# Kernel tuning notes

Measured on AMD Instinct MI355X. Metric: run time of the kernel, lower is better.

The kernel has to match this reference:

```python
import jax, jax.numpy as jnp
import numpy as np


def setup_inputs() -> dict:
    key = jax.random.key(0)
    ks = jax.random.split(key, 4)
    B, C, H, W = 16, 3, 256, 256
    n_steps, kO, k = 10, 2, 3
    CK = C * kO
    x = jax.random.normal(ks[0], (B, C, H, W), jnp.float32)
    kerK = jax.random.normal(ks[1], (n_steps, CK, 1, k, k), jnp.float32) * 0.3
    beta = jax.random.uniform(ks[2], (n_steps, 1, CK, 1, 1), jnp.float32, minval=0.01, maxval=0.1)
    rho = jax.random.uniform(ks[3], (n_steps, 1, CK, 1, 1), jnp.float32, minval=0.5, maxval=1.5)
    return {"x": x, "kerK": kerK, "beta": beta, "rho": rho}


def _dwconv(ker, x, pad):
    # depthwise 'same' cross-correlation (torch conv2d semantics)
    # ker: (CK,1,k,k), x: (B,CK,H,W) -> (B,CK,H,W)
    return jax.lax.conv_general_dilated(
        x, ker, (1, 1), [(pad, pad), (pad, pad)],
        dimension_numbers=("NCHW", "OIHW", "NCHW"),
        feature_group_count=x.shape[1])


def _psf2otf(ker, H, W):
    # ker: (C, kk, kk) with kk odd; shift center to origin, then FFT -> (C,H,W) complex
    C, kk, _ = ker.shape
    r = (kk - 1) // 2
    pad = jnp.zeros((C, H, W), ker.dtype).at[:, :kk, :kk].set(ker)
    pad = jnp.roll(pad, (-r, -r), axis=(-2, -1))
    return jnp.fft.fft2(pad)


def _tv_forward(x, kerK, beta, rho):
    B, C, H, W = x.shape
    n_steps, CK, _, k, _ = kerK.shape
    kO = CK // C
    kR = (k - 1) // 2
    f = x
    u = x                                        # state u init = input (loop(): u = x0)
    p = jnp.zeros((B, CK, H, W), x.dtype)        # auxiliary p ~= Du
    mu = jnp.zeros_like(p)                       # scaled multiplier
    for i in range(n_steps):                     # structural unroll over fixed n_steps
        K = kerK[i]                              # (CK,1,k,k)
        rh = rho[i]                              # (1,CK,1,1)
        gm = beta[i] / rho[i]                    # gamma = beta/rho (per step docstring)
        # kerW = rho * flip(K): adjoint D^T as correlation with flipped kernel
        kerW = rh.reshape(CK, 1, 1, 1) * K[:, :, ::-1, ::-1]
        # w1 = f + CKtoC(D^T (p - mu)); CKtoC sums groups of kO channels
        w1 = f + _dwconv(kerW, p - mu, kR).reshape(B, C, kO, H, W).sum(2)
        # K^T K: depthwise full autocorrelation of each kernel -> (CK, 2k-1, 2k-1)
        ktk = jax.lax.conv_general_dilated(
            K.transpose(1, 0, 2, 3), K, (1, 1), [(k - 1, k - 1)] * 2,
            dimension_numbers=("NCHW", "OIHW", "NCHW"),
            feature_group_count=CK)[0] * rh.reshape(CK, 1, 1)
        sktk = ktk.reshape(C, kO, 2 * k - 1, 2 * k - 1).sum(1)   # (C,kk,kk)
        kerH = sktk.at[:, k - 1, k - 1].add(1.0)                 # I + rho*K^T K
        otf = _psf2otf(kerH, H, W)                               # (C,H,W) complex
        # FFT Wiener-style solve: u = ifft( fft(w1) / OTF )
        u = jnp.fft.ifft2(jnp.fft.fft2(w1) / otf[None]).real
        # c = D u (depthwise corr on channel-repeated u)
        c = _dwconv(K, jnp.repeat(u, kO, axis=1), kR)
        v = c + mu
        p = jnp.sign(v) * jnp.maximum(jnp.abs(v) - gm, 0.0)      # soft-threshold
        mu = mu + c - p
    return u


def reference(x, kerK, beta, rho):
    return _tv_forward(x, kerK, beta, rho)
```

## Files before the change

### kernel.cpp

```cpp
#include <hip/hip_runtime.h>
#include <hip/hip_fp16.h>
#include <math.h>

#define BATCH 16
#define CH 3
#define CKCH 6
#define HH 256
#define WW 256
#define NSTEPS 10
#define SW 132
#define HSP (HH*SW)
#define IDX(i) ((i) ^ (((i) >> 4) & 15))

struct __align__(8) h4 { __half2 a, b; };

__device__ __forceinline__ float2 cmulf(float2 a, float2 b) {
  return make_float2(a.x * b.x - a.y * b.y, a.x * b.y + a.y * b.x);
}
__device__ __forceinline__ float4 h4tof4(h4 v) {
  float2 f0 = __half22float2(v.a), f1 = __half22float2(v.b);
  return make_float4(f0.x, f0.y, f1.x, f1.y);
}
__device__ __forceinline__ h4 f4toh4(float4 v) {
  h4 r;
  r.a = __float22half2_rn(make_float2(v.x, v.y));
  r.b = __float22half2_rn(make_float2(v.z, v.w));
  return r;
}

template <int INV, int STRIDE>
__device__ __forceinline__ void wave_fft256(float2* buf, const float2* tw, int l) {
  int pp = 0;
#pragma unroll
  for (int st = 0; st < 4; ++st) {
    int m = 1 << (2 * st);
    int r = l & (m - 1);
    int qm = l - r;
    float2 w1 = tw[qm], w2 = tw[qm + 64], w3 = tw[2 * qm];
    if (INV) { w1.y = -w1.y; w2.y = -w2.y; w3.y = -w3.y; }
    const float2* src = buf + pp * STRIDE;
    float2* dst = buf + (pp ^ 1) * STRIDE;
    float2 x0 = src[IDX(l)];
    float2 x1 = src[IDX(l + 128)];
    float2 x2 = src[IDX(l + 64)];
    float2 x3 = src[IDX(l + 192)];
    __builtin_amdgcn_wave_barrier();
    float2 aA = make_float2(x0.x + x1.x, x0.y + x1.y);
    float2 bA = cmulf(w1, make_float2(x0.x - x1.x, x0.y - x1.y));
    float2 aB = make_float2(x2.x + x3.x, x2.y + x3.y);
    float2 bB = cmulf(w2, make_float2(x2.x - x3.x, x2.y - x3.y));
    int base = 4 * qm + r;
    dst[IDX(base)]         = make_float2(aA.x + aB.x, aA.y + aB.y);
    dst[IDX(base + 2 * m)] = cmulf(w3, make_float2(aA.x - aB.x, aA.y - aB.y));
    dst[IDX(base + m)]     = make_float2(bA.x + bB.x, bA.y + bB.y);
    dst[IDX(base + 3 * m)] = cmulf(w3, make_float2(bA.x - bB.x, bA.y - bB.y));
    pp ^= 1;
    __builtin_amdgcn_wave_barrier();
  }
}

__global__ __launch_bounds__(256) void xcast_kernel(const float4* __restrict__ x,
                                                    h4* __restrict__ xh) {
  int i = blockIdx.x * 256 + threadIdx.x;
  xh[i] = f4toh4(x[i]);
}

__global__ __launch_bounds__(256) void hinv3_kernel(const float* __restrict__ kerK,
                                                    const float* __restrict__ rho,
                                                    float* __restrict__ HinvT) {
  int bid = blockIdx.x;
  int kx = bid % 129;
  int ic = bid / 129;
  int c = ic % CH, i = ic / CH;
  __shared__ float kerH[25];
  __shared__ float ctab[256];
  int tid = threadIdx.x;
  if (tid < 25) {
    int a = tid / 5, b = tid % 5;
    float s = (a == 2 && b == 2) ? 1.0f : 0.0f;
    for (int o = 0; o < 2; ++o) {
      int ck = c * 2 + o;
      const float* Kk = kerK + (i * CKCH + ck) * 9;
      float rh = rho[i * CKCH + ck];
      float ac = 0.f;
      for (int ty = 0; ty < 3; ++ty)
        for (int tx = 0; tx < 3; ++tx) {
          int ya = a - 2 + ty, xb = b - 2 + tx;
          if (ya >= 0 && ya < 3 && xb >= 0 && xb < 3)
            ac += Kk[ya * 3 + xb] * Kk[ty * 3 + tx];
        }
      s += rh * ac;
    }
    kerH[tid] = s;
  }
  ctab[tid] = cosf(6.283185307179586f * (float)tid / 256.0f);
  __syncthreads();
  int ky = tid;
  float acc = 0.f;
#pragma unroll
  for (int a = 0; a < 5; ++a)
#pragma unroll
    for (int b = 0; b < 5; ++b)
      acc += kerH[a * 5 + b] * ctab[(ky * (a - 2) + kx * (b - 2)) & 255];
  HinvT[((size_t)ic * 129 + kx) * 256 + ky] = 1.0f / (65536.0f * acc);
}

__global__ __launch_bounds__(256, 3) void bigstep_kernel(
    const __half* __restrict__ xh, const float* __restrict__ kerK,
    const float* __restrict__ beta, const float* __restrict__ rho,
    const __half2* __restrict__ specIn, const __half* __restrict__ muIn,
    __half* __restrict__ muOut, __half2* __restrict__ specOut,
    float* __restrict__ uout, int wstep) {
  int bid = blockIdx.x;
  int strip = bid & 31;
  int bc = bid >> 5;
  int c = bc % CH, b = bc / CH;
  int y0 = strip * 8;
  int tid = threadIdx.x;
  int u = tid >> 6, l = tid & 63;
  bool final_ = (wstep == 10);
  bool first = (wstep == 0);

  __shared__ float su[12][264];
  __shared__ float sd[2][10][264];
  __shared__ float2 zz[4][2][256];
  __shared__ float2 tw[128];

  if (tid < 128) {
    float sn, cs;
    sincosf(-6.283185307179586f * (float)tid / 256.0f, &sn, &cs);
    tw[tid] = make_float2(cs, sn);
  }
  __syncthreads();

  float2* Z = &zz[u][0][0];

  if (wstep >= 1) {
    int nround = final_ ? 1 : 2;
    for (int round = 0; round < nround; ++round) {
      int j = final_ ? (u + 1) : (round * 4 + u);
      bool act = (j < 6);
      int ya = y0 - 2 + 2 * j;
      if (act && ya >= 0 && ya < HH) {
        const __half2* Ar = specIn + ((size_t)bc * HH + ya) * SW;
        const __half2* Br = Ar + SW;
#pragma unroll
        for (int h = 0; h < 2; ++h) {
          int t = l + h * 64;
          float2 A = __half22float2(Ar[t]), B = __half22float2(Br[t]);
          Z[IDX(t)] = make_float2(A.x - B.y, A.y + B.x);
          int mI = 128 - t;
          float2 Am = __half22float2(Ar[mI]), Bm = __half22float2(Br[mI]);
          float2 zh;
          if (t == 0) zh = make_float2(Am.x - Bm.y, Am.y + Bm.x);
          else        zh = make_float2(Am.x + Bm.y, Bm.x - Am.y);
          Z[IDX(t + 128)] = zh;
        }
        __builtin_amdgcn_wave_barrier();
        wave_fft256<1, 256>(Z, tw, l);
        if (final_) {
          float* oa = uout + ((size_t)bc * HH + ya) * WW;
#pragma unroll
          for (int h = 0; h < 4; ++h) {
            int xx = l + h * 64;
            float2 z = Z[IDX(xx)];
            oa[xx] = z.x;
            oa[WW + xx] = z.y;
          }
        } else {
          int r0 = 2 * j;
#pragma unroll
          for (int h = 0; h < 4; ++h) {
            int xx = l + h * 64;
            float2 z = Z[IDX(xx)];
            su[r0][4 + xx] = z.x;
            su[r0 + 1][4 + xx] = z.y;
          }
        }
      } else if (act) {
        int r0 = 2 * j;
        for (int k2 = l; k2 < 264; k2 += 64) { su[r0][k2] = 0.f; su[r0 + 1][k2] = 0.f; }
      }
    }
  }
  if (final_) return;

  if (!first) {
    __syncthreads();
    bool muZero = (wstep == 1);
    int ps = wstep - 1;
#pragma unroll 1
    for (int it = 0; it < 5; ++it) {
      int task = it * 4 + u;
      int o = task / 10, rr = task % 10;
      int y = y0 - 1 + rr;
      int ck = c * 2 + o;
      float4 dq = make_float4(0.f, 0.f, 0.f, 0.f);
      if (y >= 0 && y < HH) {
        const float* Kp = kerK + (ps * CKCH + ck) * 9;
        float kk[9];
#pragma unroll
        for (int q = 0; q < 9; ++q) kk[q] = Kp[q];
        float gm = beta[ps * CKCH + ck] / rho[ps * CKCH + ck];
        float4 c4 = make_float4(0.f, 0.f, 0.f, 0.f);
#pragma unroll
        for (int dy = 0; dy < 3; ++dy) {
          float4 mid = *(const float4*)&su[rr + dy][4 + 4 * l];
          float lft = __shfl_up(mid.w, 1); if (l == 0) lft = 0.f;
          float rgt = __shfl_down(mid.x, 1); if (l == 63) rgt = 0.f;
          float w0 = kk[dy * 3], w1 = kk[dy * 3 + 1], w2 = kk[dy * 3 + 2];
          c4.x += w0 * lft   + w1 * mid.x + w2 * mid.y;
          c4.y += w0 * mid.x + w1 * mid.y + w2 * mid.z;
          c4.z += w0 * mid.y + w1 * mid.z + w2 * mid.w;
          c4.w += w0 * mid.z + w1 * mid.w + w2 * rgt;
        }
        size_t gidx = (((size_t)b * CKCH + ck) * HH + y) * WW + 4 * l;
        float4 m4 = make_float4(0.f, 0.f, 0.f, 0.f);
        if (!muZero) m4 = h4tof4(*(const h4*)(muIn + gidx));
        float4 mn4;
        {
          float v = c4.x + m4.x, av = fabsf(v) - gm;
          float pn = (av > 0.f) ? ((v > 0.f) ? av : -av) : 0.f;
          mn4.x = m4.x + c4.x - pn; dq.x = pn - mn4.x;
        }
        {
          float v = c4.y + m4.y, av = fabsf(v) - gm;
          float pn = (av > 0.f) ? ((v > 0.f) ? av : -av) : 0.f;
          mn4.y = m4.y + c4.y - pn; dq.y = pn - mn4.y;
        }
        {
          float v = c4.z + m4.z, av = fabsf(v) - gm;
          float pn = (av > 0.f) ? ((v > 0.f) ? av : -av) : 0.f;
          mn4.z = m4.z + c4.z - pn; dq.z = pn - mn4.z;
        }
        {
          float v = c4.w + m4.w, av = fabsf(v) - gm;
          float pn = (av > 0.f) ? ((v > 0.f) ? av : -av) : 0.f;
          mn4.w = m4.w + c4.w - pn; dq.w = pn - mn4.w;
        }
        if (rr >= 1 && rr <= 8) *(h4*)(muOut + gidx) = f4toh4(mn4);
      }
      *(float4*)&sd[o][rr][4 + 4 * l] = dq;
    }
  }
  __syncthreads();

  int ya = y0 + 2 * u;
  const h4* xa = (const h4*)(xh + ((size_t)(b * CH + c) * HH + ya) * WW);
  float4 va = h4tof4(xa[l]), vb = h4tof4(xa[64 + l]);
  if (!first) {
#pragma unroll
    for (int o = 0; o < 2; ++o) {
      int ck = c * 2 + o;
      float rh = rho[wstep * CKCH + ck];
      const float* Kk = kerK + (wstep * CKCH + ck) * 9;
      float kw[9];
#pragma unroll
      for (int dy = 0; dy < 3; ++dy)
#pragma unroll
        for (int dx = 0; dx < 3; ++dx)
          kw[dy * 3 + dx] = rh * Kk[(2 - dy) * 3 + (2 - dx)];
      float4 mid[4]; float lf[4], rg[4];
#pragma unroll
      for (int r4 = 0; r4 < 4; ++r4) {
        mid[r4] = *(const float4*)&sd[o][2 * u + r4][4 + 4 * l];
        lf[r4] = __shfl_up(mid[r4].w, 1); if (l == 0) lf[r4] = 0.f;
        rg[r4] = __shfl_down(mid[r4].x, 1); if (l == 63) rg[r4] = 0.f;
      }
#pragma unroll
      for (int dy = 0; dy < 3; ++dy) {
        float w0 = kw[dy * 3], w1 = kw[dy * 3 + 1], w2 = kw[dy * 3 + 2];
        va.x += w0 * lf[dy]     + w1 * mid[dy].x   + w2 * mid[dy].y;
        va.y += w0 * mid[dy].x  + w1 * mid[dy].y   + w2 * mid[dy].z;
        va.z += w0 * mid[dy].y  + w1 * mid[dy].z   + w2 * mid[dy].w;
        va.w += w0 * mid[dy].z  + w1 * mid[dy].w   + w2 * rg[dy];
        vb.x += w0 * lf[dy+1]    + w1 * mid[dy+1].x + w2 * mid[dy+1].y;
        vb.y += w0 * mid[dy+1].x + w1 * mid[dy+1].y + w2 * mid[dy+1].z;
        vb.z += w0 * mid[dy+1].y + w1 * mid[dy+1].z + w2 * mid[dy+1].w;
        vb.w += w0 * mid[dy+1].z + w1 * mid[dy+1].w + w2 * rg[dy+1];
      }
    }
  }
  Z[IDX(4 * l + 0)] = make_float2(va.x, vb.x);
  Z[IDX(4 * l + 1)] = make_float2(va.y, vb.y);
  Z[IDX(4 * l + 2)] = make_float2(va.z, vb.z);
  Z[IDX(4 * l + 3)] = make_float2(va.w, vb.w);
  __builtin_amdgcn_wave_barrier();
  wave_fft256<0, 256>(Z, tw, l);
  __half2* Sa = specOut + ((size_t)bc * HH + ya) * SW;
  __half2* Sb = Sa + SW;
#pragma unroll
  for (int h = 0; h < 2; ++h) {
    int k = l + h * 64;
    int mI = (256 - k) & 255;
    float2 zk = Z[IDX(k)], zm = Z[IDX(mI)];
    Sa[k] = __float22half2_rn(make_float2(0.5f * (zk.x + zm.x), 0.5f * (zk.y - zm.y)));
    Sb[k] = __float22half2_rn(make_float2(0.5f * (zk.y + zm.y), 0.5f * (zm.x - zk.x)));
  }
  if (l == 0) {
    float2 z1 = Z[IDX(128)];
    Sa[128] = __float22half2_rn(make_float2(z1.x, 0.f));
    Sb[128] = __float22half2_rn(make_float2(z1.y, 0.f));
  }
}

__global__ __launch_bounds__(256, 4) void colfft_kernel(__half2* __restrict__ spec,
                                                        const float* __restrict__ HinvT, int step) {
  int bid = blockIdx.x;
  int g = bid % 17;
  int bc = bid / 17;
  int c = bc % CH;
  int x0 = g * 8;
  __half2* f = spec + (size_t)bc * HSP;

  __shared__ float2 az[8][2][258];
  __shared__ float2 tw[128];
  int tid = threadIdx.x;
  if (tid < 128) {
    float sn, cs;
    sincosf(-6.283185307179586f * (float)tid / 256.0f, &sn, &cs);
    tw[tid] = make_float2(cs, sn);
  }
  for (int e = tid; e < 2048; e += 256) {
    int row = e >> 3, col = e & 7;
    int kx = x0 + col;
    if (kx <= 128) az[col][0][IDX(row)] = __half22float2(f[row * SW + kx]);
  }
  __syncthreads();

  int u = tid >> 6, l = tid & 63;
#pragma unroll
  for (int cc = 0; cc < 2; ++cc) {
    int col = 2 * u + cc;
    int kx = x0 + col;
    if (kx <= 128) {
      float2* A = &az[col][0][0];
      wave_fft256<0, 258>(A, tw, l);
      const float* T = HinvT + ((size_t)(step * CH + c) * 129 + kx) * 256;
#pragma unroll
      for (int h = 0; h < 4; ++h) {
        int idx = l + 64 * h;
        float tv = T[idx];
        float2 z = A[IDX(idx)];
        A[IDX(idx)] = make_float2(z.x * tv, z.y * tv);
      }
      __builtin_amdgcn_wave_barrier();
      wave_fft256<1, 258>(A, tw, l);
    }
  }
  __syncthreads();
  for (int e = tid; e < 2048; e += 256) {
    int row = e >> 3, col = e & 7;
    int kx = x0 + col;
    if (kx <= 128) f[row * SW + kx] = __float22half2_rn(az[col][0][IDX(row)]);
  }
}

extern "C" void kernel_launch(void* const* d_in, const int* in_sizes, int n_in,
                              void* d_out, int out_size, void* d_ws, size_t ws_size,
                              hipStream_t stream) {
  const float* x = (const float*)d_in[0];
  const float* kerK = (const float*)d_in[1];
  const float* beta = (const float*)d_in[2];
  const float* rho = (const float*)d_in[3];
  float* out = (float*)d_out;

  const size_t PMU = (size_t)BATCH * CKCH * HH * WW;
  const size_t SPL = (size_t)BATCH * CH * HSP;
  const size_t XN = (size_t)BATCH * CH * HH * WW;

  __half* muA = (__half*)d_ws;
  __half* muB = muA + PMU;
  __half2* specA = (__half2*)(muB + PMU);
  __half2* specB = specA + SPL;
  float* HinvT = (float*)(specB + SPL);
  __half* xh = (__half*)(HinvT + (size_t)30 * 129 * 256);

  xcast_kernel<<<XN / 1024, 256, 0, stream>>>((const float4*)x, (h4*)xh);
  hinv3_kernel<<<30 * 129, 256, 0, stream>>>(kerK, rho, HinvT);

  for (int i = 0; i < NSTEPS; ++i) {
    __half2* sIn = (i & 1) ? specA : specB;
    __half2* sOut = (i & 1) ? specB : specA;
    const __half* mi = (i & 1) ? muB : muA;
    __half* mo = (i & 1) ? muA : muB;
    bigstep_kernel<<<BATCH * CH * 32, 256, 0, stream>>>(
        xh, kerK, beta, rho, sIn, mi, mo, sOut, out, i);
    colfft_kernel<<<BATCH * CH * 17, 256, 0, stream>>>(sOut, HinvT, i);
  }
  bigstep_kernel<<<BATCH * CH * 32, 256, 0, stream>>>(
      xh, kerK, beta, rho, specB, muA, muB, specA, out, 10);
}
```

Before: 429.5 us.

## Shrink LDS footprint: in-place FFT, half-precision staging, one column per wave

The wave-level radix-4 FFT now works in place on a single buffer instead of ping-ponging between two, which halves the FFT scratch in both kernels. The bigstep kernel stores its u and dual staging tiles in LDS as fp16 and raises its occupancy hint. The column FFT kernel switches to 512-thread blocks with one column per wave. The aim is to cut LDS per block so more waves stay resident and hide latency, at the cost of extra fp16 rounding in intermediates. In-place updates rely on each lane reading all four inputs before the wave barrier and then writing.

```diff
diff --git a/kernel.cpp b/kernel.cpp
--- a/kernel.cpp
+++ b/kernel.cpp
@@ -28,9 +28,8 @@
   return r;
 }
 
-template <int INV, int STRIDE>
+template <int INV>
 __device__ __forceinline__ void wave_fft256(float2* buf, const float2* tw, int l) {
-  int pp = 0;
 #pragma unroll
   for (int st = 0; st < 4; ++st) {
     int m = 1 << (2 * st);
@@ -38,23 +37,20 @@
     int qm = l - r;
     float2 w1 = tw[qm], w2 = tw[qm + 64], w3 = tw[2 * qm];
     if (INV) { w1.y = -w1.y; w2.y = -w2.y; w3.y = -w3.y; }
-    const float2* src = buf + pp * STRIDE;
-    float2* dst = buf + (pp ^ 1) * STRIDE;
-    float2 x0 = src[IDX(l)];
-    float2 x1 = src[IDX(l + 128)];
-    float2 x2 = src[IDX(l + 64)];
-    float2 x3 = src[IDX(l + 192)];
+    float2 x0 = buf[IDX(l)];
+    float2 x1 = buf[IDX(l + 128)];
+    float2 x2 = buf[IDX(l + 64)];
+    float2 x3 = buf[IDX(l + 192)];
     __builtin_amdgcn_wave_barrier();
     float2 aA = make_float2(x0.x + x1.x, x0.y + x1.y);
     float2 bA = cmulf(w1, make_float2(x0.x - x1.x, x0.y - x1.y));
     float2 aB = make_float2(x2.x + x3.x, x2.y + x3.y);
     float2 bB = cmulf(w2, make_float2(x2.x - x3.x, x2.y - x3.y));
     int base = 4 * qm + r;
-    dst[IDX(base)]         = make_float2(aA.x + aB.x, aA.y + aB.y);
-    dst[IDX(base + 2 * m)] = cmulf(w3, make_float2(aA.x - aB.x, aA.y - aB.y));
-    dst[IDX(base + m)]     = make_float2(bA.x + bB.x, bA.y + bB.y);
-    dst[IDX(base + 3 * m)] = cmulf(w3, make_float2(bA.x - bB.x, bA.y - bB.y));
-    pp ^= 1;
+    buf[IDX(base)]         = make_float2(aA.x + aB.x, aA.y + aB.y);
+    buf[IDX(base + 2 * m)] = cmulf(w3, make_float2(aA.x - aB.x, aA.y - aB.y));
+    buf[IDX(base + m)]     = make_float2(bA.x + bB.x, bA.y + bB.y);
+    buf[IDX(base + 3 * m)] = cmulf(w3, make_float2(bA.x - bB.x, bA.y - bB.y));
     __builtin_amdgcn_wave_barrier();
   }
 }
@@ -105,7 +101,7 @@
   HinvT[((size_t)ic * 129 + kx) * 256 + ky] = 1.0f / (65536.0f * acc);
 }
 
-__global__ __launch_bounds__(256, 3) void bigstep_kernel(
+__global__ __launch_bounds__(256, 6) void bigstep_kernel(
     const __half* __restrict__ xh, const float* __restrict__ kerK,
     const float* __restrict__ beta, const float* __restrict__ rho,
     const __half2* __restrict__ specIn, const __half* __restrict__ muIn,
@@ -121,9 +117,9 @@
   bool final_ = (wstep == 10);
   bool first = (wstep == 0);
 
-  __shared__ float su[12][264];
-  __shared__ float sd[2][10][264];
-  __shared__ float2 zz[4][2][256];
+  __shared__ __half su[12][264];
+  __shared__ __half sdm[2][10][264];
+  __shared__ float2 zz[4][256];
   __shared__ float2 tw[128];
 
   if (tid < 128) {
@@ -133,7 +129,7 @@
   }
   __syncthreads();
 
-  float2* Z = &zz[u][0][0];
+  float2* Z = &zz[u][0];
 
   if (wstep >= 1) {
     int nround = final_ ? 1 : 2;
@@ -157,7 +153,7 @@
           Z[IDX(t + 128)] = zh;
         }
         __builtin_amdgcn_wave_barrier();
-        wave_fft256<1, 256>(Z, tw, l);
+        wave_fft256<1>(Z, tw, l);
         if (final_) {
           float* oa = uout + ((size_t)bc * HH + ya) * WW;
 #pragma unroll
@@ -173,13 +169,16 @@
           for (int h = 0; h < 4; ++h) {
             int xx = l + h * 64;
             float2 z = Z[IDX(xx)];
-            su[r0][4 + xx] = z.x;
-            su[r0 + 1][4 + xx] = z.y;
+            su[r0][4 + xx] = __float2half(z.x);
+            su[r0 + 1][4 + xx] = __float2half(z.y);
           }
         }
       } else if (act) {
         int r0 = 2 * j;
-        for (int k2 = l; k2 < 264; k2 += 64) { su[r0][k2] = 0.f; su[r0 + 1][k2] = 0.f; }
+        for (int k2 = l; k2 < 264; k2 += 64) {
+          su[r0][k2] = __float2half(0.f);
+          su[r0 + 1][k2] = __float2half(0.f);
+        }
       }
     }
   }
@@ -205,7 +204,7 @@
         float4 c4 = make_float4(0.f, 0.f, 0.f, 0.f);
 #pragma unroll
         for (int dy = 0; dy < 3; ++dy) {
-          float4 mid = *(const float4*)&su[rr + dy][4 + 4 * l];
+          float4 mid = h4tof4(*(const h4*)&su[rr + dy][4 + 4 * l]);
           float lft = __shfl_up(mid.w, 1); if (l == 0) lft = 0.f;
           float rgt = __shfl_down(mid.x, 1); if (l == 63) rgt = 0.f;
           float w0 = kk[dy * 3], w1 = kk[dy * 3 + 1], w2 = kk[dy * 3 + 2];
@@ -240,7 +239,7 @@
         }
         if (rr >= 1 && rr <= 8) *(h4*)(muOut + gidx) = f4toh4(mn4);
       }
-      *(float4*)&sd[o][rr][4 + 4 * l] = dq;
+      *(h4*)&sdm[o][rr][4 + 4 * l] = f4toh4(dq);
     }
   }
   __syncthreads();
@@ -263,7 +262,7 @@
       float4 mid[4]; float lf[4], rg[4];
 #pragma unroll
       for (int r4 = 0; r4 < 4; ++r4) {
-        mid[r4] = *(const float4*)&sd[o][2 * u + r4][4 + 4 * l];
+        mid[r4] = h4tof4(*(const h4*)&sdm[o][2 * u + r4][4 + 4 * l]);
         lf[r4] = __shfl_up(mid[r4].w, 1); if (l == 0) lf[r4] = 0.f;
         rg[r4] = __shfl_down(mid[r4].x, 1); if (l == 63) rg[r4] = 0.f;
       }
@@ -286,7 +285,7 @@
   Z[IDX(4 * l + 2)] = make_float2(va.z, vb.z);
   Z[IDX(4 * l + 3)] = make_float2(va.w, vb.w);
   __builtin_amdgcn_wave_barrier();
-  wave_fft256<0, 256>(Z, tw, l);
+  wave_fft256<0>(Z, tw, l);
   __half2* Sa = specOut + ((size_t)bc * HH + ya) * SW;
   __half2* Sb = Sa + SW;
 #pragma unroll
@@ -304,7 +303,7 @@
   }
 }
 
-__global__ __launch_bounds__(256, 4) void colfft_kernel(__half2* __restrict__ spec,
+__global__ __launch_bounds__(512, 6) void colfft_kernel(__half2* __restrict__ spec,
                                                         const float* __restrict__ HinvT, int step) {
   int bid = blockIdx.x;
   int g = bid % 17;
@@ -313,7 +312,7 @@
   int x0 = g * 8;
   __half2* f = spec + (size_t)bc * HSP;
 
-  __shared__ float2 az[8][2][258];
+  __shared__ float2 az[8][258];
   __shared__ float2 tw[128];
   int tid = threadIdx.x;
   if (tid < 128) {
@@ -321,38 +320,34 @@
     sincosf(-6.283185307179586f * (float)tid / 256.0f, &sn, &cs);
     tw[tid] = make_float2(cs, sn);
   }
-  for (int e = tid; e < 2048; e += 256) {
+  for (int e = tid; e < 2048; e += 512) {
     int row = e >> 3, col = e & 7;
     int kx = x0 + col;
-    if (kx <= 128) az[col][0][IDX(row)] = __half22float2(f[row * SW + kx]);
+    if (kx <= 128) az[col][IDX(row)] = __half22float2(f[row * SW + kx]);
   }
   __syncthreads();
 
   int u = tid >> 6, l = tid & 63;
-#pragma unroll
-  for (int cc = 0; cc < 2; ++cc) {
-    int col = 2 * u + cc;
-    int kx = x0 + col;
-    if (kx <= 128) {
-      float2* A = &az[col][0][0];
-      wave_fft256<0, 258>(A, tw, l);
-      const float* T = HinvT + ((size_t)(step * CH + c) * 129 + kx) * 256;
-#pragma unroll
-      for (int h = 0; h < 4; ++h) {
-        int idx = l + 64 * h;
-        float tv = T[idx];
-        float2 z = A[IDX(idx)];
-        A[IDX(idx)] = make_float2(z.x * tv, z.y * tv);
-      }
-      __builtin_amdgcn_wave_barrier();
-      wave_fft256<1, 258>(A, tw, l);
-    }
-  }
-  __syncthreads();
-  for (int e = tid; e < 2048; e += 256) {
+  int kx = x0 + u;
+  if (kx <= 128) {
+    float2* A = &az[u][0];
+    wave_fft256<0>(A, tw, l);
+    const float* T = HinvT + ((size_t)(step * CH + c) * 129 + kx) * 256;
+#pragma unroll
+    for (int h = 0; h < 4; ++h) {
+      int idx = l + 64 * h;
+      float tv = T[idx];
+      float2 z = A[IDX(idx)];
+      A[IDX(idx)] = make_float2(z.x * tv, z.y * tv);
+    }
+    __builtin_amdgcn_wave_barrier();
+    wave_fft256<1>(A, tw, l);
+  }
+  __syncthreads();
+  for (int e = tid; e < 2048; e += 512) {
     int row = e >> 3, col = e & 7;
-    int kx = x0 + col;
-    if (kx <= 128) f[row * SW + kx] = __float22half2_rn(az[col][0][IDX(row)]);
+    int kx2 = x0 + col;
+    if (kx2 <= 128) f[row * SW + kx2] = __float22half2_rn(az[col][IDX(row)]);
   }
 }
 
@@ -386,7 +381,7 @@
     __half* mo = (i & 1) ? muA : muB;
     bigstep_kernel<<<BATCH * CH * 32, 256, 0, stream>>>(
         xh, kerK, beta, rho, sIn, mi, mo, sOut, out, i);
-    colfft_kernel<<<BATCH * CH * 17, 256, 0, stream>>>(sOut, HinvT, i);
+    colfft_kernel<<<BATCH * CH * 17, 512, 0, stream>>>(sOut, HinvT, i);
   }
   bigstep_kernel<<<BATCH * CH * 32, 256, 0, stream>>>(
       xh, kerK, beta, rho, specB, muA, muB, specA, out, 10);
```

Result: faster. 415.0 us (-3.4%).
